# Kernel optimization log

Measured on AMD Instinct MI355X. Metric: run time of the kernel, lower is better.

Reference implementation:

```python
import jax, jax.numpy as jnp
import numpy as np

NUM_HEADS = 8
HIDDEN = 8

def conv1x1(x, w):
    # x: [B,C,H,W], w: [O,C] -> [B,O,H,W]
    return jnp.einsum('oc,bchw->bohw', w, x)

def grid_sample_border(img, gx, gy):
    # Bilinear grid_sample, padding_mode='border', align_corners=True.
    # img: [B,C,H,W]; gx, gy: [B,H,W] normalized coords in [-1,1].
    B, C, H, W = img.shape
    ix = (gx + 1.0) * 0.5 * (W - 1)
    iy = (gy + 1.0) * 0.5 * (H - 1)
    x0f = jnp.floor(ix); y0f = jnp.floor(iy)
    wx = (ix - x0f)[..., None]; wy = (iy - y0f)[..., None]
    x0 = x0f.astype(jnp.int32); y0 = y0f.astype(jnp.int32)
    x0c = jnp.clip(x0, 0, W - 1); x1c = jnp.clip(x0 + 1, 0, W - 1)
    y0c = jnp.clip(y0, 0, H - 1); y1c = jnp.clip(y0 + 1, 0, H - 1)
    imt = jnp.transpose(img, (0, 2, 3, 1))  # [B,H,W,C]
    b = jnp.arange(B)[:, None, None]
    v00 = imt[b, y0c, x0c]; v01 = imt[b, y0c, x1c]
    v10 = imt[b, y1c, x0c]; v11 = imt[b, y1c, x1c]
    out = (v00 * (1 - wx) * (1 - wy) + v01 * wx * (1 - wy)
           + v10 * (1 - wx) * wy + v11 * wx * wy)
    return jnp.transpose(out, (0, 3, 1, 2))

def process_sub(cur, ref, Wq, Wk, Wv, Wver, Whor):
    B, C, H, W = cur.shape
    c = HIDDEN // NUM_HEADS  # per-head channel dim (=1)
    q = conv1x1(cur, Wq).reshape(B, NUM_HEADS, c, H, W)
    k = conv1x1(ref, Wk).reshape(B, NUM_HEADS, c, H, W)
    v = conv1x1(ref, Wv).reshape(B, NUM_HEADS, c, H, W)
    # vertical axial attention (each column w independent, attend over rows)
    a_ver = jax.nn.softmax(jnp.einsum('bkchw,bkclw->bkwhl', q, k), axis=-1)
    o_ver = jnp.einsum('bkwhl,bkclw->bkchw', a_ver, v).reshape(B, HIDDEN, H, W)
    o_ver = conv1x1(o_ver, Wver)[:, 0]  # [B,H,W]
    # horizontal axial attention (each row h independent, attend over cols)
    a_hor = jax.nn.softmax(jnp.einsum('bkchw,bkchl->bkhwl', q, k), axis=-1)
    o_hor = jnp.einsum('bkhwl,bkchl->bkchw', a_hor, v).reshape(B, HIDDEN, H, W)
    o_hor = conv1x1(o_hor, Whor)[:, 0]  # [B,H,W]
    # identity grid + flow
    ys = -1.0 + 2.0 * jnp.arange(H, dtype=cur.dtype) / max(float(H - 1), 1.0)
    xs = -1.0 + 2.0 * jnp.arange(W, dtype=cur.dtype) / max(float(W - 1), 1.0)
    gx = xs[None, None, :] + o_hor / ((W - 1.0) / 2.0)
    gy = ys[None, :, None] + o_ver / ((H - 1.0) / 2.0)
    return grid_sample_border(ref, gx, gy)

def _forward(cur_fea, ref_fea, Wq, Wk, Wv, Wver, Whor):
    B, C, H, W = cur_fea.shape
    def split(x):
        return jnp.stack([x[:, :, ::2, ::2], x[:, :, 1::2, 1::2],
                          x[:, :, ::2, 1::2], x[:, :, 1::2, ::2]], 0)
    cur_sub = split(cur_fea).reshape(4 * B, C, H // 2, W // 2)
    ref_sub = split(ref_fea).reshape(4 * B, C, H // 2, W // 2)
    warped = process_sub(cur_sub, ref_sub, Wq, Wk, Wv, Wver, Whor)
    ul, br, ur, bl = warped.reshape(4, B, C, H // 2, W // 2)
    out = jnp.zeros((B, C, H, W), dtype=jnp.float32)
    out = out.at[:, :, ::2, ::2].set(ul)
    out = out.at[:, :, ::2, 1::2].set(ur)
    out = out.at[:, :, 1::2, ::2].set(bl)
    out = out.at[:, :, 1::2, 1::2].set(br)
    return out

def setup_inputs() -> dict:
    key = jax.random.key(0)
    ks = jax.random.split(key, 7)
    B, C, H, W = 2, 64, 256, 256
    return {
        'cur_fea': jax.random.normal(ks[0], (B, C, H, W), jnp.float32),
        'ref_fea': jax.random.normal(ks[1], (B, C, H, W), jnp.float32),
        'Wq': jax.random.normal(ks[2], (HIDDEN, C), jnp.float32) * 0.05,
        'Wk': jax.random.normal(ks[3], (HIDDEN, C), jnp.float32) * 0.05,
        'Wv': jax.random.normal(ks[4], (HIDDEN, C), jnp.float32) * 0.05,
        'Wver': jax.random.normal(ks[5], (1, HIDDEN), jnp.float32) * 0.05,
        'Whor': jax.random.normal(ks[6], (1, HIDDEN), jnp.float32) * 0.05,
    }

def reference(cur_fea, ref_fea, Wq, Wk, Wv, Wver, Whor):
    return _forward(cur_fea, ref_fea, Wq, Wk, Wv, Wver, Whor)
```

## Files before the change

kernel.cpp:

```cpp
#include <hip/hip_runtime.h>


constexpr int PLANE = 16384;
constexpr float LOG2E = 1.4426950408889634f;

__global__ __launch_bounds__(512) void qkv_kernel(
    const float* __restrict__ cur, const float* __restrict__ ref,
    const float* __restrict__ Wq, const float* __restrict__ Wk,
    const float* __restrict__ Wv,
    float* __restrict__ Q, float* __restrict__ K, float* __restrict__ V)
{
    __shared__ float WT[64 * 24];
    __shared__ float red0[128 * 25];
    __shared__ float red1[128 * 25];
    const int tid = threadIdx.x;
    for (int i = tid; i < 64 * 24; i += 512) {
        int c = i / 24, j = i % 24;
        float val = (j < 8) ? Wq[j * 64 + c]
                  : (j < 16) ? Wk[(j - 8) * 64 + c]
                  : Wv[(j - 16) * 64 + c];
        WT[c * 24 + j] = val;
    }
    __syncthreads();

    const int bi = blockIdx.x;
    const int b  = bi >> 9;
    const int Y  = (bi >> 1) & 255;
    const int Xh = bi & 1;
    const int cg = tid >> 7;
    const int xi = tid & 127;
    const int X  = Xh * 128 + xi;

    const size_t base_in = (size_t)b * 64 * 65536 + (size_t)Y * 256 + X;
    const float* curp = cur + base_in;
    const float* refp = ref + base_in;

    float q[8], k[8], v[8];
#pragma unroll
    for (int i = 0; i < 8; ++i) { q[i] = 0.f; k[i] = 0.f; v[i] = 0.f; }

    const int c0 = cg * 16;
#pragma unroll 8
    for (int c = 0; c < 16; ++c) {
        float cu = curp[(size_t)(c0 + c) * 65536];
        float rf = refp[(size_t)(c0 + c) * 65536];
        const float* wr = &WT[(c0 + c) * 24];
#pragma unroll
        for (int i = 0; i < 8; ++i) {
            q[i] = fmaf(wr[i],      cu, q[i]);
            k[i] = fmaf(wr[8 + i],  rf, k[i]);
            v[i] = fmaf(wr[16 + i], rf, v[i]);
        }
    }

    float* row0 = &red0[xi * 25];
    float* row1 = &red1[xi * 25];
    if (cg == 1) {
#pragma unroll
        for (int i = 0; i < 8; ++i) {
            row0[i] = q[i]; row0[8 + i] = k[i]; row0[16 + i] = v[i];
        }
    } else if (cg == 3) {
#pragma unroll
        for (int i = 0; i < 8; ++i) {
            row1[i] = q[i]; row1[8 + i] = k[i]; row1[16 + i] = v[i];
        }
    }
    __syncthreads();
    if (cg == 2) {
#pragma unroll
        for (int i = 0; i < 8; ++i) {
            row1[i]      += q[i];
            row1[8 + i]  += k[i];
            row1[16 + i] += v[i];
        }
    } else if (cg == 0) {
#pragma unroll
        for (int i = 0; i < 8; ++i) {
            q[i] += row0[i]; k[i] += row0[8 + i]; v[i] += row0[16 + i];
        }
    }
    __syncthreads();
    if (cg == 0) {
        const int dy = Y & 1, dx = X & 1;
        const int p  = dy ? (dx ? 1 : 3) : (dx ? 2 : 0);
        const int sb = p * 2 + b;
        const int h = Y >> 1, w = X >> 1;
#pragma unroll
        for (int i = 0; i < 8; ++i) {
            const size_t o = ((size_t)(sb * 8 + i) << 14) + (h << 7) + w;
            Q[o] = q[i] + row1[i];
            K[o] = k[i] + row1[8 + i];
            V[o] = v[i] + row1[16 + i];
        }
    }
}

__global__ __launch_bounds__(256) void transpose_kernel(
    const float* __restrict__ Q, const float* __restrict__ K,
    const float* __restrict__ V,
    float* __restrict__ QT, float* __restrict__ KT, float* __restrict__ VT)
{
    __shared__ float tile[32 * 33];
    const int bi = blockIdx.x;
    const int plane = bi >> 4;
    const int ti = (bi >> 2) & 3, tj = bi & 3;
    const int t = threadIdx.x;
    const int r = t >> 3, c4 = (t & 7) * 4;
    const size_t pb = (size_t)plane << 14;
    const size_t ibase = pb + (size_t)(ti * 32) * 128 + tj * 32;
    const size_t obase = pb + (size_t)(tj * 32) * 128 + ti * 32;

    const float* srcs[3] = { Q, K, V };
    float* dsts[3] = { QT, KT, VT };
#pragma unroll
    for (int a = 0; a < 3; ++a) {
        const float* src = srcs[a];
        float* dst = dsts[a];
        const float4 val = *(const float4*)&src[ibase + (size_t)r * 128 + c4];
        if (a) __syncthreads();
        tile[r * 33 + c4 + 0] = val.x;
        tile[r * 33 + c4 + 1] = val.y;
        tile[r * 33 + c4 + 2] = val.z;
        tile[r * 33 + c4 + 3] = val.w;
        __syncthreads();
        float4 o;
        o.x = tile[(c4 + 0) * 33 + r];
        o.y = tile[(c4 + 1) * 33 + r];
        o.z = tile[(c4 + 2) * 33 + r];
        o.w = tile[(c4 + 3) * 33 + r];
        *(float4*)&dst[obase + (size_t)r * 128 + c4] = o;
    }
}

__global__ __launch_bounds__(256) void attn_fused(
    const float* __restrict__ Q, const float* __restrict__ K,
    const float* __restrict__ V,
    const float* __restrict__ QT, const float* __restrict__ KT,
    const float* __restrict__ VT,
    const float* __restrict__ Whor, const float* __restrict__ Wver,
    float* __restrict__ OH, float* __restrict__ OVT)
{
    __shared__ float kk[8 * 128];
    __shared__ float vv[8 * 128];
    __shared__ float red[8 * 128];

    const int pass = blockIdx.x >> 10;
    const float* __restrict__ Qa = pass ? QT : Q;
    const float* __restrict__ Ka = pass ? KT : K;
    const float* __restrict__ Va = pass ? VT : V;
    const float* __restrict__ wsel = pass ? Wver : Whor;
    float* __restrict__ o = pass ? OVT : OH;

    const int tid  = threadIdx.x;
    const int sub  = tid >> 7;
    const int t    = tid & 127;
    const int sbl  = blockIdx.x & 1023;
    const int sb   = sbl >> 7;
    const int line = sbl & 127;

    const size_t base = (((size_t)(sb * 8)) << 14) + ((size_t)line << 7);
#pragma unroll
    for (int i = 0; i < 4; ++i) {
        const int idx = i * 256 + tid;
        const int hh = idx >> 7, tt = idx & 127;
        const size_t g = base + ((size_t)hh << 14) + tt;
        kk[idx] = LOG2E * Ka[g];
        vv[idx] = Va[g];
    }
    __syncthreads();

#pragma unroll
    for (int i = 0; i < 4; ++i) {
        const int head = sub * 4 + i;
        const float s = Qa[base + ((size_t)head << 14) + t];
        const float4* k4 = (const float4*)&kk[head << 7];
        const float4* v4 = (const float4*)&vv[head << 7];
        float d0 = 0.f, d1 = 0.f, d2 = 0.f, d3 = 0.f;
        float n0 = 0.f, n1 = 0.f, n2 = 0.f, n3 = 0.f;
#pragma unroll 8
        for (int l = 0; l < 32; ++l) {
            const float4 kq = k4[l];
            const float4 vq = v4[l];
            const float e0 = __builtin_amdgcn_exp2f(s * kq.x);
            const float e1 = __builtin_amdgcn_exp2f(s * kq.y);
            const float e2 = __builtin_amdgcn_exp2f(s * kq.z);
            const float e3 = __builtin_amdgcn_exp2f(s * kq.w);
            d0 += e0; n0 = fmaf(e0, vq.x, n0);
            d1 += e1; n1 = fmaf(e1, vq.y, n1);
            d2 += e2; n2 = fmaf(e2, vq.z, n2);
            d3 += e3; n3 = fmaf(e3, vq.w, n3);
        }
        const float den = (d0 + d1) + (d2 + d3);
        const float num = (n0 + n1) + (n2 + n3);
        red[(head << 7) + t] = num * __builtin_amdgcn_rcpf(den);
    }
    __syncthreads();

    if (tid < 128) {
        float acc = 0.f;
#pragma unroll
        for (int i = 0; i < 8; ++i)
            acc = fmaf(wsel[i], red[(i << 7) + tid], acc);
        o[((size_t)sb << 14) + ((size_t)line << 7) + tid] = acc;
    }
}

__global__ __launch_bounds__(256) void warp_kernel(
    const float* __restrict__ ref, const float* __restrict__ ovt,
    const float* __restrict__ oh, float* __restrict__ out)
{
    const int bi = blockIdx.x;
    const int Y  = bi & 255;
    const int cg = (bi >> 8) & 3;
    const int b  = bi >> 10;
    const int X  = threadIdx.x;

    const int dy = Y & 1, dx = X & 1;
    const int p  = dy ? (dx ? 1 : 3) : (dx ? 2 : 0);
    const int sb = p * 2 + b;
    const int h = Y >> 1, w = X >> 1;

    const float ix = (float)w + oh [((size_t)sb << 14) + (h << 7) + w];
    const float iy = (float)h + ovt[((size_t)sb << 14) + (w << 7) + h];

    const float x0f = floorf(ix), y0f = floorf(iy);
    const float wx = ix - x0f,    wy = iy - y0f;
    const int x0 = (int)x0f, y0 = (int)y0f;
    const int x0c = min(max(x0, 0), 127),     x1c = min(max(x0 + 1, 0), 127);
    const int y0c = min(max(y0, 0), 127),     y1c = min(max(y0 + 1, 0), 127);

    const float w00 = (1.f - wx) * (1.f - wy);
    const float w01 = wx * (1.f - wy);
    const float w10 = (1.f - wx) * wy;
    const float w11 = wx * wy;

    const int r0 = (2 * y0c + dy) * 256, r1 = (2 * y1c + dy) * 256;
    const int c0 = 2 * x0c + dx,         c1 = 2 * x1c + dx;
    const int o00 = r0 + c0, o01 = r0 + c1, o10 = r1 + c0, o11 = r1 + c1;
    const int dst = Y * 256 + X;

    const float* rp = ref + ((size_t)b * 64 + cg * 16) * 65536;
    float* op = out + ((size_t)b * 64 + cg * 16) * 65536;

#pragma unroll 4
    for (int c = 0; c < 16; ++c) {
        const size_t pl = (size_t)c * 65536;
        const float v00 = rp[pl + o00], v01 = rp[pl + o01];
        const float v10 = rp[pl + o10], v11 = rp[pl + o11];
        op[pl + dst] = fmaf(w00, v00, fmaf(w01, v01, fmaf(w10, v10, w11 * v11)));
    }
}

extern "C" void kernel_launch(void* const* d_in, const int* in_sizes, int n_in,
                              void* d_out, int out_size, void* d_ws, size_t ws_size,
                              hipStream_t stream)
{
    const float* cur  = (const float*)d_in[0];
    const float* ref  = (const float*)d_in[1];
    const float* Wq   = (const float*)d_in[2];
    const float* Wk   = (const float*)d_in[3];
    const float* Wv   = (const float*)d_in[4];
    const float* Wver = (const float*)d_in[5];
    const float* Whor = (const float*)d_in[6];
    float* out = (float*)d_out;

    float* ws = (float*)d_ws;
    const size_t NQ = 8 * 8 * (size_t)PLANE;
    float* Q   = ws;
    float* K   = Q  + NQ;
    float* V   = K  + NQ;
    float* QT  = V  + NQ;
    float* KT  = QT + NQ;
    float* VT  = KT + NQ;
    float* OVT = VT + NQ;
    float* OH  = OVT + 8 * (size_t)PLANE;

    qkv_kernel<<<1024, 512, 0, stream>>>(cur, ref, Wq, Wk, Wv, Q, K, V);
    transpose_kernel<<<1024, 256, 0, stream>>>(Q, K, V, QT, KT, VT);
    attn_fused<<<2048, 256, 0, stream>>>(Q, K, V, QT, KT, VT,
                                         Whor, Wver, OH, OVT);
    warp_kernel<<<2048, 256, 0, stream>>>(ref, OVT, OH, out);
}
```

Measured before the change: 196.4 us.

## Fold LOG2E into Wk, vectorize attention loads/math, fuse head reduction, float4 warp gathers

Moves the LOG2E scaling of K into the projection weights, loads K/V tiles into shared memory with float4, and uses packed two-wide float math in the softmax loop. The per-head output projection is accumulated in registers with a two-way shared reduction, replacing the 8x128 scratch buffer. The warp kernel fetches each bilinear row pair with one float4 load and selects the parity lanes, cutting four scalar gathers per channel to two vector loads. This adds select logic and relies on 16-byte alignment of the gather address.

Measured after the change: 186.2 us. 1.05x faster.

```diff
diff --git a/kernel.cpp b/kernel.cpp
--- a/kernel.cpp
+++ b/kernel.cpp
@@ -3,6 +3,8 @@
 
 constexpr int PLANE = 16384;
 constexpr float LOG2E = 1.4426950408889634f;
+
+typedef float v2f __attribute__((ext_vector_type(2)));
 
 __global__ __launch_bounds__(512) void qkv_kernel(
     const float* __restrict__ cur, const float* __restrict__ ref,
@@ -17,7 +19,7 @@
     for (int i = tid; i < 64 * 24; i += 512) {
         int c = i / 24, j = i % 24;
         float val = (j < 8) ? Wq[j * 64 + c]
-                  : (j < 16) ? Wk[(j - 8) * 64 + c]
+                  : (j < 16) ? LOG2E * Wk[(j - 8) * 64 + c]
                   : Wv[(j - 16) * 64 + c];
         WT[c * 24 + j] = val;
     }
@@ -141,9 +143,9 @@
     const float* __restrict__ Whor, const float* __restrict__ Wver,
     float* __restrict__ OH, float* __restrict__ OVT)
 {
-    __shared__ float kk[8 * 128];
-    __shared__ float vv[8 * 128];
-    __shared__ float red[8 * 128];
+    __shared__ __align__(16) float kk[8 * 128];
+    __shared__ __align__(16) float vv[8 * 128];
+    __shared__ float part[128];
 
     const int pass = blockIdx.x >> 10;
     const float* __restrict__ Qa = pass ? QT : Q;
@@ -160,49 +162,48 @@
     const int line = sbl & 127;
 
     const size_t base = (((size_t)(sb * 8)) << 14) + ((size_t)line << 7);
-#pragma unroll
-    for (int i = 0; i < 4; ++i) {
-        const int idx = i * 256 + tid;
-        const int hh = idx >> 7, tt = idx & 127;
+    {
+        const int f  = tid;
+        const int hh = f >> 5;
+        const int tt = (f & 31) << 2;
         const size_t g = base + ((size_t)hh << 14) + tt;
-        kk[idx] = LOG2E * Ka[g];
-        vv[idx] = Va[g];
-    }
-    __syncthreads();
-
+        ((float4*)kk)[f] = *(const float4*)&Ka[g];
+        ((float4*)vv)[f] = *(const float4*)&Va[g];
+    }
+    __syncthreads();
+
+    float acc = 0.f;
 #pragma unroll
     for (int i = 0; i < 4; ++i) {
         const int head = sub * 4 + i;
         const float s = Qa[base + ((size_t)head << 14) + t];
         const float4* k4 = (const float4*)&kk[head << 7];
         const float4* v4 = (const float4*)&vv[head << 7];
-        float d0 = 0.f, d1 = 0.f, d2 = 0.f, d3 = 0.f;
-        float n0 = 0.f, n1 = 0.f, n2 = 0.f, n3 = 0.f;
+        v2f d01 = {0.f, 0.f}, d23 = {0.f, 0.f};
+        v2f n01 = {0.f, 0.f}, n23 = {0.f, 0.f};
 #pragma unroll 8
         for (int l = 0; l < 32; ++l) {
             const float4 kq = k4[l];
             const float4 vq = v4[l];
-            const float e0 = __builtin_amdgcn_exp2f(s * kq.x);
-            const float e1 = __builtin_amdgcn_exp2f(s * kq.y);
-            const float e2 = __builtin_amdgcn_exp2f(s * kq.z);
-            const float e3 = __builtin_amdgcn_exp2f(s * kq.w);
-            d0 += e0; n0 = fmaf(e0, vq.x, n0);
-            d1 += e1; n1 = fmaf(e1, vq.y, n1);
-            d2 += e2; n2 = fmaf(e2, vq.z, n2);
-            d3 += e3; n3 = fmaf(e3, vq.w, n3);
-        }
-        const float den = (d0 + d1) + (d2 + d3);
-        const float num = (n0 + n1) + (n2 + n3);
-        red[(head << 7) + t] = num * __builtin_amdgcn_rcpf(den);
-    }
-    __syncthreads();
-
-    if (tid < 128) {
-        float acc = 0.f;
-#pragma unroll
-        for (int i = 0; i < 8; ++i)
-            acc = fmaf(wsel[i], red[(i << 7) + tid], acc);
-        o[((size_t)sb << 14) + ((size_t)line << 7) + tid] = acc;
+            v2f a01 = {s * kq.x, s * kq.y};
+            v2f a23 = {s * kq.z, s * kq.w};
+            v2f e01 = {__builtin_amdgcn_exp2f(a01.x), __builtin_amdgcn_exp2f(a01.y)};
+            v2f e23 = {__builtin_amdgcn_exp2f(a23.x), __builtin_amdgcn_exp2f(a23.y)};
+            d01 += e01;
+            d23 += e23;
+            n01 += e01 * (v2f){vq.x, vq.y};
+            n23 += e23 * (v2f){vq.z, vq.w};
+        }
+        const v2f dv = d01 + d23, nv = n01 + n23;
+        const float den = dv.x + dv.y;
+        const float num = nv.x + nv.y;
+        acc = fmaf(wsel[head], num * __builtin_amdgcn_rcpf(den), acc);
+    }
+
+    if (sub) part[t] = acc;
+    __syncthreads();
+    if (!sub) {
+        o[((size_t)sb << 14) + ((size_t)line << 7) + t] = acc + part[t];
     }
 }
 
@@ -235,9 +236,10 @@
     const float w10 = (1.f - wx) * wy;
     const float w11 = wx * wy;
 
+    const int cb  = min(2 * x0c, 252);
+    const bool hi  = (x0c == 127);
+    const bool up1 = hi | (x1c != x0c);
     const int r0 = (2 * y0c + dy) * 256, r1 = (2 * y1c + dy) * 256;
-    const int c0 = 2 * x0c + dx,         c1 = 2 * x1c + dx;
-    const int o00 = r0 + c0, o01 = r0 + c1, o10 = r1 + c0, o11 = r1 + c1;
     const int dst = Y * 256 + X;
 
     const float* rp = ref + ((size_t)b * 64 + cg * 16) * 65536;
@@ -246,8 +248,12 @@
 #pragma unroll 4
     for (int c = 0; c < 16; ++c) {
         const size_t pl = (size_t)c * 65536;
-        const float v00 = rp[pl + o00], v01 = rp[pl + o01];
-        const float v10 = rp[pl + o10], v11 = rp[pl + o11];
+        const float4 f0 = *(const float4*)&rp[pl + r0 + cb];
+        const float4 f1 = *(const float4*)&rp[pl + r1 + cb];
+        const float L0 = dx ? f0.y : f0.x, H0 = dx ? f0.w : f0.z;
+        const float L1 = dx ? f1.y : f1.x, H1 = dx ? f1.w : f1.z;
+        const float v00 = hi ? H0 : L0,  v01 = up1 ? H0 : L0;
+        const float v10 = hi ? H1 : L1,  v11 = up1 ? H1 : L1;
         op[pl + dst] = fmaf(w00, v00, fmaf(w01, v01, fmaf(w10, v10, w11 * v11)));
     }
 }
```
